# Optimization experiments

Measured on AMD Instinct MI355X. Metric: run time of the kernel, lower is better.

## Reference

```python
import jax, jax.numpy as jnp
import numpy as np

B, S, H, NH = 4, 1024, 2048, 16
D = H // NH  # head_dim = 128


def setup_inputs() -> dict:
    key = jax.random.key(0)
    ks = jax.random.split(key, 10)
    # RoPE tables: angle[t, j] = t * 10000^(-2j/D), cos/sin of the complex freqs_cis
    t = jnp.arange(S, dtype=jnp.float32)
    inv_freq = 1.0 / (10000.0 ** (jnp.arange(0, D, 2, dtype=jnp.float32) / D))
    ang = t[:, None] * inv_freq[None, :]  # [S, D//2]
    w = 0.02
    return {
        "hidden_states": jax.random.normal(ks[0], (B, S, H), jnp.float32),
        "freqs_cos": jnp.cos(ang),
        "freqs_sin": jnp.sin(ang),
        "attention_mask": jnp.ones((B, 1, 1, S), jnp.float32),
        "Wq": jax.random.normal(ks[1], (H, H), jnp.float32) * w,
        "bq": jnp.zeros((H,), jnp.float32),
        "Wk": jax.random.normal(ks[2], (H, H), jnp.float32) * w,
        "bk": jnp.zeros((H,), jnp.float32),
        "Wv": jax.random.normal(ks[3], (H, H), jnp.float32) * w,
        "bv": jnp.zeros((H,), jnp.float32),
        "Wo": jax.random.normal(ks[4], (H, H), jnp.float32) * w,
        "bo": jnp.zeros((H,), jnp.float32),
    }


def _rope(x, cos, sin):
    # x: [B, S, NH, D]; cos/sin: [S, D//2]. Complex multiply on (even, odd) pairs.
    x2 = x.reshape(x.shape[:-1] + (D // 2, 2))
    x0, x1 = x2[..., 0], x2[..., 1]
    c = cos[None, :, None, :]
    s = sin[None, :, None, :]
    o0 = x0 * c - x1 * s
    o1 = x0 * s + x1 * c
    return jnp.stack([o0, o1], axis=-1).reshape(x.shape)


def reference(hidden_states, freqs_cos, freqs_sin, attention_mask,
              Wq, bq, Wk, bk, Wv, bv, Wo, bo):
    b, s, _ = hidden_states.shape
    q = (hidden_states @ Wq.T + bq).reshape(b, s, NH, D)
    k = (hidden_states @ Wk.T + bk).reshape(b, s, NH, D)
    v = (hidden_states @ Wv.T + bv).reshape(b, s, NH, D)
    q = _rope(q, freqs_cos, freqs_sin)
    k = _rope(k, freqs_cos, freqs_sin)
    # scores: [b, h, q, k]; original scales by sqrt(embed_dim)=sqrt(hidden_size)
    scores = jnp.einsum('bqhd,bkhd->bhqk', q, k) / jnp.sqrt(jnp.float32(H))
    scores = jnp.where(attention_mask == 0, jnp.float32(-1e9), scores)
    probs = jax.nn.softmax(scores, axis=-1)  # dropout is identity in eval
    ctx = jnp.einsum('bhqk,bkhd->bqhd', probs, v).reshape(b, s, H)
    return ctx @ Wo.T + bo
```

## Files before the change

### kernel.cpp

```cpp
#include <hip/hip_runtime.h>
#include <stdint.h>

#define BATCH 4
#define SEQ   1024
#define NHEAD 16
#define DHEAD 128
#define HDIM  2048
#define GM    4096
#define GN    2048
#define GK    2048

typedef __attribute__((ext_vector_type(8)))  short    short8;
typedef __attribute__((ext_vector_type(4)))  float    f32x4;
typedef __attribute__((ext_vector_type(16))) float    f32x16;
typedef __attribute__((ext_vector_type(4)))  uint32_t u32x4;

__device__ __forceinline__ uint16_t f2bf(float f) {
  uint32_t u = __builtin_bit_cast(uint32_t, f);
  u += 0x7fffu + ((u >> 16) & 1u);
  return (uint16_t)(u >> 16);
}
__device__ __forceinline__ float bf2f(uint16_t h) {
  return __builtin_bit_cast(float, (uint32_t)h << 16);
}
__device__ __forceinline__ uint32_t cvtpk(float lo, float hi) {
  uint32_t r;
  asm("v_cvt_pk_bf16_f32 %0, %1, %2" : "=v"(r) : "v"(lo), "v"(hi));
  return r;
}

__device__ __forceinline__ uint32_t swz128(uint32_t a) { return a ^ (((a >> 7) & 7u) << 4); }
__device__ __forceinline__ uint32_t swz256(uint32_t a) { return a ^ (((a >> 8) & 7u) << 4); }

#define GAS __attribute__((address_space(1)))
#define LAS __attribute__((address_space(3)))
__device__ __forceinline__ void gload_lds16(const void* g, void* l) {
  __builtin_amdgcn_global_load_lds((GAS const void*)g, (LAS void*)l, 16, 0, 0);
}

__global__ void cvt_kernel(const float* __restrict__ in, uint16_t* __restrict__ out, int n8) {
  int i = blockIdx.x * 256 + threadIdx.x;
  if (i >= n8) return;
  const float4* p = (const float4*)in + (size_t)i * 2;
  float4 a = p[0], b = p[1];
  uint32_t w0 = f2bf(a.x) | ((uint32_t)f2bf(a.y) << 16);
  uint32_t w1 = f2bf(a.z) | ((uint32_t)f2bf(a.w) << 16);
  uint32_t w2 = f2bf(b.x) | ((uint32_t)f2bf(b.y) << 16);
  uint32_t w3 = f2bf(b.z) | ((uint32_t)f2bf(b.w) << 16);
  int4 r; r.x = (int)w0; r.y = (int)w1; r.z = (int)w2; r.w = (int)w3;
  *(int4*)(out + (size_t)i * 8) = r;
}

__global__ void cvtw_kernel(const float* __restrict__ W0, const float* __restrict__ W1,
                            const float* __restrict__ W2, const float* __restrict__ W3,
                            uint16_t* __restrict__ out) {
  const float* src = (blockIdx.y == 0) ? W0 : (blockIdx.y == 1) ? W1 : (blockIdx.y == 2) ? W2 : W3;
  int i = blockIdx.x * 256 + threadIdx.x;
  const float4* p = (const float4*)src + (size_t)i * 2;
  float4 a = p[0], b = p[1];
  uint32_t w0 = f2bf(a.x) | ((uint32_t)f2bf(a.y) << 16);
  uint32_t w1 = f2bf(a.z) | ((uint32_t)f2bf(a.w) << 16);
  uint32_t w2 = f2bf(b.x) | ((uint32_t)f2bf(b.y) << 16);
  uint32_t w3 = f2bf(b.z) | ((uint32_t)f2bf(b.w) << 16);
  int4 r; r.x = (int)w0; r.y = (int)w1; r.z = (int)w2; r.w = (int)w3;
  *(int4*)(out + (size_t)blockIdx.y * HDIM * HDIM + (size_t)i * 8) = r;
}

__global__ void rope_kernel(uint16_t* __restrict__ qb, uint16_t* __restrict__ kb,
                            const float* __restrict__ fcos, const float* __restrict__ fsin) {
  uint32_t i = blockIdx.x * 256 + threadIdx.x;
  uint16_t* p = (blockIdx.y == 0 ? qb : kb) + (size_t)i * 8;
  uint32_t e0 = i * 8;
  uint32_t row = e0 >> 11;
  uint32_t col = e0 & 2047;
  uint32_t s = row & (SEQ - 1);
  uint32_t pi = (col & (DHEAD - 1)) >> 1;
  float4 cv = *(const float4*)(fcos + (size_t)s * 64 + pi);
  float4 sv = *(const float4*)(fsin + (size_t)s * 64 + pi);
  int4 raw = *(const int4*)p;
  uint16_t u[8]; *(int4*)u = raw;
  float cc[4] = {cv.x, cv.y, cv.z, cv.w}, ss[4] = {sv.x, sv.y, sv.z, sv.w};
#pragma unroll
  for (int t = 0; t < 4; ++t) {
    float x0 = bf2f(u[2 * t]), x1 = bf2f(u[2 * t + 1]);
    float o0 = x0 * cc[t] - x1 * ss[t];
    float o1 = x0 * ss[t] + x1 * cc[t];
    u[2 * t] = f2bf(o0); u[2 * t + 1] = f2bf(o1);
  }
  *(int4*)p = *(int4*)u;
}

template <int MODE>
__device__ __forceinline__ void gemm_body(const uint16_t* __restrict__ A,
                                          const uint16_t* __restrict__ Bw,
                                          const float* __restrict__ bias,
                                          void* __restrict__ Cout) {
  __shared__ __align__(16) char smA[128 * 128];
  __shared__ __align__(16) char smB[128 * 128];
  const int tid = threadIdx.x, lane = tid & 63, wid = tid >> 6;
  const int c = lane & 15, g = lane >> 4;
  const int row0 = blockIdx.x * 128, col0 = blockIdx.y * 128;
  const int wr = wid >> 1, wc = wid & 1;
  f32x4 acc[4][4] = {};
  const uint32_t oBase = wid * 4096 + lane * 16;

  for (int kk = 0; kk < GK; kk += 64) {
#pragma unroll
    for (int q = 0; q < 4; ++q) {
      uint32_t o = oBase + q * 1024;
      uint32_t r = o >> 7;
      uint32_t cb = (o & 127) ^ ((r & 7u) << 4);
      gload_lds16((const char*)A + ((size_t)(row0 + r) * GK + kk) * 2 + cb,
                  smA + wid * 4096 + q * 1024);
      gload_lds16((const char*)Bw + ((size_t)(col0 + r) * GK + kk) * 2 + cb,
                  smB + wid * 4096 + q * 1024);
    }
    __syncthreads();
    short8 af[4][2], bf[4][2];
#pragma unroll
    for (int m = 0; m < 4; ++m) {
      const uint32_t row = (uint32_t)(wr * 64 + m * 16 + c);
#pragma unroll
      for (int ks = 0; ks < 2; ++ks)
        af[m][ks] = *(const short8*)(smA + row * 128 + (((uint32_t)(ks * 64 + g * 16)) ^ ((row & 7u) << 4)));
    }
#pragma unroll
    for (int n = 0; n < 4; ++n) {
      const uint32_t row = (uint32_t)(wc * 64 + n * 16 + c);
#pragma unroll
      for (int ks = 0; ks < 2; ++ks)
        bf[n][ks] = *(const short8*)(smB + row * 128 + (((uint32_t)(ks * 64 + g * 16)) ^ ((row & 7u) << 4)));
    }
#pragma unroll
    for (int m = 0; m < 4; ++m)
#pragma unroll
      for (int n = 0; n < 4; ++n)
#pragma unroll
        for (int ks = 0; ks < 2; ++ks)
          acc[m][n] = __builtin_amdgcn_mfma_f32_16x16x32_bf16(af[m][ks], bf[n][ks], acc[m][n], 0, 0, 0);
    __syncthreads();
  }

  float bn[4];
#pragma unroll
  for (int n = 0; n < 4; ++n) bn[n] = bias[col0 + wc * 64 + n * 16 + c];
#pragma unroll
  for (int m = 0; m < 4; ++m) {
    const int gr = row0 + wr * 64 + m * 16 + g * 4;
#pragma unroll
    for (int n = 0; n < 4; ++n) {
      const int gc = col0 + wc * 64 + n * 16 + c;
#pragma unroll
      for (int jj = 0; jj < 4; ++jj) {
        float v = acc[m][n][jj] + bn[n];
        if (MODE == 1) ((float*)Cout)[(size_t)(gr + jj) * GN + gc] = v;
        else           ((uint16_t*)Cout)[(size_t)(gr + jj) * GN + gc] = f2bf(v);
      }
    }
  }
}

__global__ __launch_bounds__(256, 2) void gemm_qkv_kernel(
    const uint16_t* __restrict__ X,
    const uint16_t* __restrict__ Wq, const uint16_t* __restrict__ Wk, const uint16_t* __restrict__ Wv,
    const float* __restrict__ bq, const float* __restrict__ bk, const float* __restrict__ bv,
    uint16_t* __restrict__ qo, uint16_t* __restrict__ ko, uint16_t* __restrict__ vo) {
  const uint16_t* W; const float* bias; uint16_t* out;
  if (blockIdx.z == 0)      { W = Wq; bias = bq; out = qo; }
  else if (blockIdx.z == 1) { W = Wk; bias = bk; out = ko; }
  else                      { W = Wv; bias = bv; out = vo; }
  gemm_body<0>(X, W, bias, out);
}

__global__ __launch_bounds__(256, 2) void gemm_out_kernel(
    const uint16_t* __restrict__ ctx, const uint16_t* __restrict__ Wo,
    const float* __restrict__ bo, float* __restrict__ out) {
  gemm_body<1>(ctx, Wo, bo, out);
}

__global__ __launch_bounds__(256, 2) void attn_kernel(
    const uint16_t* __restrict__ q, const uint16_t* __restrict__ k,
    const uint16_t* __restrict__ v, const float* __restrict__ mask,
    uint16_t* __restrict__ ctx) {
  __shared__ __align__(16) char pool[33024];
  char* smK  = pool;
  char* smVT = pool + 16384;
  float* smMaskF = (float*)(pool + 32768);
  float* smT = (float*)pool;

  const int tid = threadIdx.x, lane = tid & 63, wid = tid >> 6;
  const int c32 = lane & 31, hi = lane >> 5;
  const int lb = (blockIdx.x & 7) * 64 + (blockIdx.x >> 3);
  const int qt = lb & 7, bh = lb >> 3;
  const int h = bh & (NHEAD - 1), b = bh >> 4;
  const int q0 = qt * 128;
  const float scale = 0.022097086912079608f;

  short8 qreg[8];
  {
    const uint16_t* qrow = q + (size_t)(b * SEQ + q0 + wid * 32 + c32) * HDIM + h * DHEAD;
#pragma unroll
    for (int ks = 0; ks < 8; ++ks) qreg[ks] = *(const short8*)(qrow + ks * 16 + hi * 8);
  }

  const int kvg = tid >> 5;
  const int d0v = (tid & 31) * 4;

  float mreg = -1e30f, lreg = 0.f;
  f32x16 o[4] = {};

  for (int t = 0; t < 16; ++t) {
    const int kv0 = t * 64;
    __syncthreads();
#pragma unroll
    for (int i = 0; i < 4; ++i) {
      uint32_t o_ = wid * 4096 + i * 1024 + lane * 16;
      uint32_t r = o_ >> 8;
      uint32_t cb = swz256(o_) & 255;
      gload_lds16((const char*)k + ((size_t)(b * SEQ + kv0 + r) * HDIM + h * DHEAD) * 2 + cb,
                  smK + wid * 4096 + i * 1024);
    }
    if (tid < 64) smMaskF[tid] = mask[b * SEQ + kv0 + tid];
    {
      const uint16_t* vsrc = v + (size_t)(b * SEQ + kv0 + kvg * 8) * HDIM + h * DHEAD + d0v;
      uint32_t vw[8][2];
#pragma unroll
      for (int e = 0; e < 8; ++e) {
        uint2 t2 = *(const uint2*)(vsrc + (size_t)e * HDIM);
        vw[e][0] = t2.x; vw[e][1] = t2.y;
      }
#pragma unroll
      for (int j = 0; j < 4; ++j) {
        const int hw = j >> 1, sh = (j & 1) * 16;
        int4 pk;
        pk.x = (int)(((vw[0][hw] >> sh) & 0xffffu) | (((vw[1][hw] >> sh) & 0xffffu) << 16));
        pk.y = (int)(((vw[2][hw] >> sh) & 0xffffu) | (((vw[3][hw] >> sh) & 0xffffu) << 16));
        pk.z = (int)(((vw[4][hw] >> sh) & 0xffffu) | (((vw[5][hw] >> sh) & 0xffffu) << 16));
        pk.w = (int)(((vw[6][hw] >> sh) & 0xffffu) | (((vw[7][hw] >> sh) & 0xffffu) << 16));
        *(int4*)(smVT + swz128((uint32_t)((d0v + j) * 128 + kvg * 16))) = pk;
      }
    }
    __syncthreads();

    f32x16 st[2] = {};
#pragma unroll
    for (int ks = 0; ks < 8; ++ks) {
#pragma unroll
      for (int mi = 0; mi < 2; ++mi) {
        const uint32_t row = (uint32_t)(mi * 32 + c32);
        short8 kf = *(const short8*)(smK + row * 256 +
                    (((uint32_t)(ks * 32 + hi * 16)) ^ ((row & 7u) << 4)));
        st[mi] = __builtin_amdgcn_mfma_f32_32x32x16_bf16(kf, qreg[ks], st[mi], 0, 0, 0);
      }
    }

    float p[32];
    float pmax = -1e30f;
#pragma unroll
    for (int mi = 0; mi < 2; ++mi) {
      const float* mb = smMaskF + mi * 32 + hi * 4;
      float4 m0 = *(const float4*)(mb);
      float4 m1 = *(const float4*)(mb + 8);
      float4 m2 = *(const float4*)(mb + 16);
      float4 m3 = *(const float4*)(mb + 24);
      float mm[16] = {m0.x, m0.y, m0.z, m0.w, m1.x, m1.y, m1.z, m1.w,
                      m2.x, m2.y, m2.z, m2.w, m3.x, m3.y, m3.z, m3.w};
#pragma unroll
      for (int r = 0; r < 16; ++r) {
        float s = st[mi][r] * scale;
        if (mm[r] == 0.f) s = -1e9f;
        p[mi * 16 + r] = s;
        pmax = fmaxf(pmax, s);
      }
    }
    pmax = fmaxf(pmax, __shfl_xor(pmax, 32, 64));

    if (!__all(pmax <= mreg + 8.f)) {
      float mnew = fmaxf(mreg, pmax);
      float fac = __expf(mreg - mnew);
      lreg *= fac;
#pragma unroll
      for (int dt = 0; dt < 4; ++dt)
#pragma unroll
        for (int e = 0; e < 16; ++e) o[dt][e] *= fac;
      mreg = mnew;
    }

    float rsum = 0.f;
    short8 pfrag[4];
#pragma unroll
    for (int mi = 0; mi < 2; ++mi) {
      float pe[16];
#pragma unroll
      for (int r = 0; r < 16; ++r) {
        pe[r] = __expf(p[mi * 16 + r] - mreg);
        rsum += pe[r];
      }
      uint32_t w[8], s[8];
#pragma unroll
      for (int j = 0; j < 8; ++j) w[j] = cvtpk(pe[2 * j], pe[2 * j + 1]);
#pragma unroll
      for (int j = 0; j < 8; ++j) s[j] = (uint32_t)__shfl_xor((int)w[j], 32, 64);
      u32x4 f0, f1;
      f0[0] = hi ? s[2] : w[0];  f0[1] = hi ? s[3] : w[1];
      f0[2] = hi ? w[2] : s[0];  f0[3] = hi ? w[3] : s[1];
      f1[0] = hi ? s[6] : w[4];  f1[1] = hi ? s[7] : w[5];
      f1[2] = hi ? w[6] : s[4];  f1[3] = hi ? w[7] : s[5];
      pfrag[mi * 2]     = __builtin_bit_cast(short8, f0);
      pfrag[mi * 2 + 1] = __builtin_bit_cast(short8, f1);
    }
    rsum += __shfl_xor(rsum, 32, 64);
    lreg += rsum;

#pragma unroll
    for (int dt = 0; dt < 4; ++dt) {
      const uint32_t row = (uint32_t)(dt * 32 + c32);
#pragma unroll
      for (int e = 0; e < 4; ++e) {
        short8 vf = *(const short8*)(smVT + row * 128 +
                    (((uint32_t)(e * 32 + hi * 16)) ^ ((row & 7u) << 4)));
        o[dt] = __builtin_amdgcn_mfma_f32_32x32x16_bf16(vf, pfrag[e], o[dt], 0, 0, 0);
      }
    }
  }

  const float linv = 1.f / lreg;
  float* myT = smT + wid * (32 * 36);
  const int qe = lane >> 1, de0 = (lane & 1) * 16;
#pragma unroll
  for (int dt = 0; dt < 4; ++dt) {
    __syncthreads();
#pragma unroll
    for (int r = 0; r < 16; ++r) {
      const int drow = (r & 3) + 8 * (r >> 2) + 4 * hi;
      myT[c32 * 36 + drow] = o[dt][r] * linv;
    }
    asm volatile("s_waitcnt lgkmcnt(0)" ::: "memory");
    float vv[16];
#pragma unroll
    for (int j = 0; j < 4; ++j) {
      float4 rd = *(const float4*)(myT + qe * 36 + de0 + j * 4);
      vv[j * 4 + 0] = rd.x; vv[j * 4 + 1] = rd.y; vv[j * 4 + 2] = rd.z; vv[j * 4 + 3] = rd.w;
    }
    uint32_t pw[8];
#pragma unroll
    for (int m = 0; m < 8; ++m)
      pw[m] = f2bf(vv[2 * m]) | ((uint32_t)f2bf(vv[2 * m + 1]) << 16);
    uint16_t* dst = ctx + (size_t)(b * SEQ + q0 + wid * 32 + qe) * HDIM + h * DHEAD + dt * 32 + de0;
    int4 s0; s0.x = (int)pw[0]; s0.y = (int)pw[1]; s0.z = (int)pw[2]; s0.w = (int)pw[3];
    int4 s1; s1.x = (int)pw[4]; s1.y = (int)pw[5]; s1.z = (int)pw[6]; s1.w = (int)pw[7];
    *(int4*)(dst) = s0;
    *(int4*)(dst + 8) = s1;
  }
}

extern "C" void kernel_launch(void* const* d_in, const int* in_sizes, int n_in,
                              void* d_out, int out_size, void* d_ws, size_t ws_size,
                              hipStream_t stream) {
  const float* hs   = (const float*)d_in[0];
  const float* fcos = (const float*)d_in[1];
  const float* fsin = (const float*)d_in[2];
  const float* mask = (const float*)d_in[3];
  const float* Wq = (const float*)d_in[4];  const float* bq = (const float*)d_in[5];
  const float* Wk = (const float*)d_in[6];  const float* bk = (const float*)d_in[7];
  const float* Wv = (const float*)d_in[8];  const float* bv = (const float*)d_in[9];
  const float* Wo = (const float*)d_in[10]; const float* bo = (const float*)d_in[11];
  float* out = (float*)d_out;

  char* ws = (char*)d_ws;
  const size_t XB = (size_t)GM * HDIM * 2;
  const size_t WB = (size_t)HDIM * HDIM * 2;
  uint16_t* Xbf = (uint16_t*)(ws);
  uint16_t* Wqb = (uint16_t*)(ws + XB);
  uint16_t* Wkb = (uint16_t*)(ws + XB + WB);
  uint16_t* Wvb = (uint16_t*)(ws + XB + 2 * WB);
  uint16_t* Wob = (uint16_t*)(ws + XB + 3 * WB);
  uint16_t* qb  = (uint16_t*)(ws + XB + 4 * WB);
  uint16_t* kb  = (uint16_t*)(ws + XB + 4 * WB + XB);
  uint16_t* vb  = (uint16_t*)(ws + XB + 4 * WB + 2 * XB);

  cvt_kernel<<<4096, 256, 0, stream>>>(hs, Xbf, (GM * HDIM) / 8);
  cvtw_kernel<<<dim3(2048, 4), 256, 0, stream>>>(Wq, Wk, Wv, Wo, Wqb);

  gemm_qkv_kernel<<<dim3(GM / 128, GN / 128, 3), 256, 0, stream>>>(
      Xbf, Wqb, Wkb, Wvb, bq, bk, bv, qb, kb, vb);

  rope_kernel<<<dim3((GM * HDIM) / 8 / 256, 2, 1), 256, 0, stream>>>(qb, kb, fcos, fsin);

  attn_kernel<<<512, 256, 0, stream>>>(qb, kb, vb, mask, Xbf);

  gemm_out_kernel<<<dim3(GM / 128, GN / 128, 1), 256, 0, stream>>>(Xbf, Wob, bo, out);
}
```

Baseline: 243.3 us.

## Double-buffer K/V tiles in attention and merge conversion kernels into one

The attention kernel now double-buffers the K, transposed-V and mask tiles in LDS. The next tile's global loads are issued before the QK^T MFMAs, and its LDS writes happen after the softmax, which overlaps memory latency with compute and removes one barrier per iteration. LDS use doubles to about 66KB per block, which may limit occupancy under launch_bounds(256,2). The separate activation and weight fp32-to-bf16 conversion kernels are merged into one launch to save launch overhead. The epilogue drops its per-tile barrier, relying on each wave writing only its own private transpose region.

After: 240.9 us. About the same (-1.0%).

```diff
diff --git a/kernel.cpp b/kernel.cpp
--- a/kernel.cpp
+++ b/kernel.cpp
@@ -38,32 +38,30 @@
   __builtin_amdgcn_global_load_lds((GAS const void*)g, (LAS void*)l, 16, 0, 0);
 }
 
-__global__ void cvt_kernel(const float* __restrict__ in, uint16_t* __restrict__ out, int n8) {
-  int i = blockIdx.x * 256 + threadIdx.x;
-  if (i >= n8) return;
-  const float4* p = (const float4*)in + (size_t)i * 2;
+__global__ void cvt_all_kernel(const float* __restrict__ hs,
+                               const float* __restrict__ W0, const float* __restrict__ W1,
+                               const float* __restrict__ W2, const float* __restrict__ W3,
+                               uint16_t* __restrict__ Xbf, uint16_t* __restrict__ Wb) {
+  const int bid = blockIdx.x;
+  const float* src; uint16_t* dst;
+  if (bid < 4096) {
+    src = hs + (size_t)bid * 2048;
+    dst = Xbf + (size_t)bid * 2048;
+  } else {
+    const int m = (bid - 4096) >> 11;
+    const int blk = (bid - 4096) & 2047;
+    const float* Ws = (m == 0) ? W0 : (m == 1) ? W1 : (m == 2) ? W2 : W3;
+    src = Ws + (size_t)blk * 2048;
+    dst = Wb + (size_t)m * HDIM * HDIM + (size_t)blk * 2048;
+  }
+  const float4* p = (const float4*)src + (size_t)threadIdx.x * 2;
   float4 a = p[0], b = p[1];
   uint32_t w0 = f2bf(a.x) | ((uint32_t)f2bf(a.y) << 16);
   uint32_t w1 = f2bf(a.z) | ((uint32_t)f2bf(a.w) << 16);
   uint32_t w2 = f2bf(b.x) | ((uint32_t)f2bf(b.y) << 16);
   uint32_t w3 = f2bf(b.z) | ((uint32_t)f2bf(b.w) << 16);
   int4 r; r.x = (int)w0; r.y = (int)w1; r.z = (int)w2; r.w = (int)w3;
-  *(int4*)(out + (size_t)i * 8) = r;
-}
-
-__global__ void cvtw_kernel(const float* __restrict__ W0, const float* __restrict__ W1,
-                            const float* __restrict__ W2, const float* __restrict__ W3,
-                            uint16_t* __restrict__ out) {
-  const float* src = (blockIdx.y == 0) ? W0 : (blockIdx.y == 1) ? W1 : (blockIdx.y == 2) ? W2 : W3;
-  int i = blockIdx.x * 256 + threadIdx.x;
-  const float4* p = (const float4*)src + (size_t)i * 2;
-  float4 a = p[0], b = p[1];
-  uint32_t w0 = f2bf(a.x) | ((uint32_t)f2bf(a.y) << 16);
-  uint32_t w1 = f2bf(a.z) | ((uint32_t)f2bf(a.w) << 16);
-  uint32_t w2 = f2bf(b.x) | ((uint32_t)f2bf(b.y) << 16);
-  uint32_t w3 = f2bf(b.z) | ((uint32_t)f2bf(b.w) << 16);
-  int4 r; r.x = (int)w0; r.y = (int)w1; r.z = (int)w2; r.w = (int)w3;
-  *(int4*)(out + (size_t)blockIdx.y * HDIM * HDIM + (size_t)i * 8) = r;
+  *(int4*)(dst + (size_t)threadIdx.x * 8) = r;
 }
 
 __global__ void rope_kernel(uint16_t* __restrict__ qb, uint16_t* __restrict__ kb,
@@ -182,10 +180,7 @@
     const uint16_t* __restrict__ q, const uint16_t* __restrict__ k,
     const uint16_t* __restrict__ v, const float* __restrict__ mask,
     uint16_t* __restrict__ ctx) {
-  __shared__ __align__(16) char pool[33024];
-  char* smK  = pool;
-  char* smVT = pool + 16384;
-  float* smMaskF = (float*)(pool + 32768);
+  __shared__ __align__(16) char pool[66048];
   float* smT = (float*)pool;
 
   const int tid = threadIdx.x, lane = tid & 63, wid = tid >> 6;
@@ -206,41 +201,66 @@
   const int kvg = tid >> 5;
   const int d0v = (tid & 31) * 4;
 
-  float mreg = -1e30f, lreg = 0.f;
-  f32x16 o[4] = {};
-
-  for (int t = 0; t < 16; ++t) {
-    const int kv0 = t * 64;
-    __syncthreads();
+  auto issueK = [&](int s) {
+    char* dK = pool + (s & 1) * 16384;
 #pragma unroll
     for (int i = 0; i < 4; ++i) {
       uint32_t o_ = wid * 4096 + i * 1024 + lane * 16;
       uint32_t r = o_ >> 8;
       uint32_t cb = swz256(o_) & 255;
-      gload_lds16((const char*)k + ((size_t)(b * SEQ + kv0 + r) * HDIM + h * DHEAD) * 2 + cb,
-                  smK + wid * 4096 + i * 1024);
-    }
-    if (tid < 64) smMaskF[tid] = mask[b * SEQ + kv0 + tid];
-    {
-      const uint16_t* vsrc = v + (size_t)(b * SEQ + kv0 + kvg * 8) * HDIM + h * DHEAD + d0v;
-      uint32_t vw[8][2];
-#pragma unroll
-      for (int e = 0; e < 8; ++e) {
-        uint2 t2 = *(const uint2*)(vsrc + (size_t)e * HDIM);
-        vw[e][0] = t2.x; vw[e][1] = t2.y;
-      }
-#pragma unroll
-      for (int j = 0; j < 4; ++j) {
-        const int hw = j >> 1, sh = (j & 1) * 16;
-        int4 pk;
-        pk.x = (int)(((vw[0][hw] >> sh) & 0xffffu) | (((vw[1][hw] >> sh) & 0xffffu) << 16));
-        pk.y = (int)(((vw[2][hw] >> sh) & 0xffffu) | (((vw[3][hw] >> sh) & 0xffffu) << 16));
-        pk.z = (int)(((vw[4][hw] >> sh) & 0xffffu) | (((vw[5][hw] >> sh) & 0xffffu) << 16));
-        pk.w = (int)(((vw[6][hw] >> sh) & 0xffffu) | (((vw[7][hw] >> sh) & 0xffffu) << 16));
-        *(int4*)(smVT + swz128((uint32_t)((d0v + j) * 128 + kvg * 16))) = pk;
-      }
-    }
-    __syncthreads();
+      gload_lds16((const char*)k + ((size_t)(b * SEQ + s * 64 + r) * HDIM + h * DHEAD) * 2 + cb,
+                  dK + wid * 4096 + i * 1024);
+    }
+  };
+  auto loadV = [&](int s, uint32_t vw[8][2]) {
+    const uint16_t* vsrc = v + (size_t)(b * SEQ + s * 64 + kvg * 8) * HDIM + h * DHEAD + d0v;
+#pragma unroll
+    for (int e = 0; e < 8; ++e) {
+      uint2 t2 = *(const uint2*)(vsrc + (size_t)e * HDIM);
+      vw[e][0] = t2.x; vw[e][1] = t2.y;
+    }
+  };
+  auto writeVT = [&](int s, uint32_t vw[8][2]) {
+    char* dVT = pool + 32768 + (s & 1) * 16384;
+#pragma unroll
+    for (int j = 0; j < 4; ++j) {
+      const int hw = j >> 1, sh = (j & 1) * 16;
+      int4 pk;
+      pk.x = (int)(((vw[0][hw] >> sh) & 0xffffu) | (((vw[1][hw] >> sh) & 0xffffu) << 16));
+      pk.y = (int)(((vw[2][hw] >> sh) & 0xffffu) | (((vw[3][hw] >> sh) & 0xffffu) << 16));
+      pk.z = (int)(((vw[4][hw] >> sh) & 0xffffu) | (((vw[5][hw] >> sh) & 0xffffu) << 16));
+      pk.w = (int)(((vw[6][hw] >> sh) & 0xffffu) | (((vw[7][hw] >> sh) & 0xffffu) << 16));
+      *(int4*)(dVT + swz128((uint32_t)((d0v + j) * 128 + kvg * 16))) = pk;
+    }
+  };
+
+  float mreg = -1e30f, lreg = 0.f;
+  f32x16 o[4] = {};
+
+  {
+    float mtmp = 0.f;
+    if (tid < 64) mtmp = mask[b * SEQ + tid];
+    uint32_t vw[8][2];
+    loadV(0, vw);
+    issueK(0);
+    if (tid < 64) ((float*)(pool + 65536))[tid] = mtmp;
+    writeVT(0, vw);
+  }
+  __syncthreads();
+
+  for (int t = 0; t < 16; ++t) {
+    const int cur = t & 1;
+    const char* sK  = pool + cur * 16384;
+    const char* sVT = pool + 32768 + cur * 16384;
+    const float* smMaskF = (const float*)(pool + 65536 + cur * 256);
+
+    float mtmp = 0.f;
+    uint32_t vw[8][2];
+    if (t < 15) {
+      if (tid < 64) mtmp = mask[b * SEQ + (t + 1) * 64 + tid];
+      loadV(t + 1, vw);
+      issueK(t + 1);
+    }
 
     f32x16 st[2] = {};
 #pragma unroll
@@ -248,7 +268,7 @@
 #pragma unroll
       for (int mi = 0; mi < 2; ++mi) {
         const uint32_t row = (uint32_t)(mi * 32 + c32);
-        short8 kf = *(const short8*)(smK + row * 256 +
+        short8 kf = *(const short8*)(sK + row * 256 +
                     (((uint32_t)(ks * 32 + hi * 16)) ^ ((row & 7u) << 4)));
         st[mi] = __builtin_amdgcn_mfma_f32_32x32x16_bf16(kf, qreg[ks], st[mi], 0, 0, 0);
       }
@@ -312,16 +332,23 @@
     rsum += __shfl_xor(rsum, 32, 64);
     lreg += rsum;
 
+    if (t < 15) {
+      if (tid < 64) ((float*)(pool + 65536 + ((t + 1) & 1) * 256))[tid] = mtmp;
+      writeVT(t + 1, vw);
+    }
+
 #pragma unroll
     for (int dt = 0; dt < 4; ++dt) {
       const uint32_t row = (uint32_t)(dt * 32 + c32);
 #pragma unroll
       for (int e = 0; e < 4; ++e) {
-        short8 vf = *(const short8*)(smVT + row * 128 +
+        short8 vf = *(const short8*)(sVT + row * 128 +
                     (((uint32_t)(e * 32 + hi * 16)) ^ ((row & 7u) << 4)));
         o[dt] = __builtin_amdgcn_mfma_f32_32x32x16_bf16(vf, pfrag[e], o[dt], 0, 0, 0);
       }
     }
+
+    __syncthreads();
   }
 
   const float linv = 1.f / lreg;
@@ -329,13 +356,11 @@
   const int qe = lane >> 1, de0 = (lane & 1) * 16;
 #pragma unroll
   for (int dt = 0; dt < 4; ++dt) {
-    __syncthreads();
 #pragma unroll
     for (int r = 0; r < 16; ++r) {
       const int drow = (r & 3) + 8 * (r >> 2) + 4 * hi;
       myT[c32 * 36 + drow] = o[dt][r] * linv;
     }
-    asm volatile("s_waitcnt lgkmcnt(0)" ::: "memory");
     float vv[16];
 #pragma unroll
     for (int j = 0; j < 4; ++j) {
@@ -379,8 +404,7 @@
   uint16_t* kb  = (uint16_t*)(ws + XB + 4 * WB + XB);
   uint16_t* vb  = (uint16_t*)(ws + XB + 4 * WB + 2 * XB);
 
-  cvt_kernel<<<4096, 256, 0, stream>>>(hs, Xbf, (GM * HDIM) / 8);
-  cvtw_kernel<<<dim3(2048, 4), 256, 0, stream>>>(Wq, Wk, Wv, Wo, Wqb);
+  cvt_all_kernel<<<12288, 256, 0, stream>>>(hs, Wq, Wk, Wv, Wo, Xbf, Wqb);
 
   gemm_qkv_kernel<<<dim3(GM / 128, GN / 128, 3), 256, 0, stream>>>(
       Xbf, Wqb, Wkb, Wvb, bq, bk, bv, qb, kb, vb);
```
